# Kernel tuning notes

Hardware: AMD Instinct MI355X
Metric: run time of the kernel (lower is better)

## Reference

```python
import jax, jax.numpy as jnp
import numpy as np


def setup_inputs() -> dict:
    key = jax.random.key(0)
    x = jax.random.normal(key, (8, 16, 256, 256, 3, 3), dtype=jnp.float32)
    return {"x": x, "padding_dim": 1}


def reference(x, padding_dim):
    """Vectorized SPD identity-pad: borders get eye(3), interior copies x.

    x: [B, C, H, W, 3, 3] -> [B, C, H+2p, W+2p, 3, 3]
    Faithful to the original quadruple-nested-loop `padding` function.
    """
    p = padding_dim
    B, C, H, W = x.shape[:4]
    # zero-pad spatial dims, then overwrite border cells with identity
    xp = jnp.pad(x, ((0, 0), (0, 0), (p, p), (p, p), (0, 0), (0, 0)))
    row = jnp.arange(H + 2 * p)
    col = jnp.arange(W + 2 * p)
    # border condition matches: i < p or (H+2p - i) <= p  (i.e. i >= H+p)
    row_border = (row < p) | (row >= H + p)          # [H+2p]
    col_border = (col < p) | (col >= W + p)          # [W+2p]
    border = row_border[:, None] | col_border[None, :]  # [H+2p, W+2p]
    eye = jnp.eye(3, dtype=x.dtype)
    out = jnp.where(border[None, None, :, :, None, None], eye, xp)
    return out
```

## Files before the change

### kernel.cpp

```cpp
#include <hip/hip_runtime.h>


constexpr int B  = 8;
constexpr int C  = 16;
constexpr int H  = 256;
constexpr int W  = 256;
constexpr int HP = 258;
constexpr int WP = 258;

constexpr int       IMGS    = B * C;
constexpr long long ROW_IN  = (long long)W * 9;
constexpr long long IMG_IN  = (long long)H * ROW_IN;
constexpr long long ROW_OUT = (long long)WP * 9;
constexpr long long IMG_OUT = (long long)HP * ROW_OUT;

constexpr int COPY_BLOCKS   = IMGS * H;
constexpr int BORDER_BLOCKS = 2048;
constexpr int       CELLS_PER_IMG = 2 * WP + 2 * H;
constexpr long long BORDER_FLOATS = (long long)IMGS * CELLS_PER_IMG * 9;

__global__ __launch_bounds__(192) void spd_pad_kernel(const float* __restrict__ x,
                                                      float* __restrict__ out) {
    const int blk = blockIdx.x;
    const int tid = threadIdx.x;

    if (blk < COPY_BLOCKS) {
        const int img = blk >> 8;
        const int i   = blk & 255;
        const float4* __restrict__ src =
            reinterpret_cast<const float4*>(x + (long long)img * IMG_IN + (long long)i * ROW_IN);
        float4* __restrict__ dst =
            reinterpret_cast<float4*>(out + (long long)img * IMG_OUT + (long long)(i + 1) * ROW_OUT + 9);
#pragma unroll
        for (int k = 0; k < 3; ++k) {
            const int idx = tid + k * 192;
            dst[idx] = src[idx];
        }
    } else {
        const long long stride = (long long)BORDER_BLOCKS * 192;
        long long t = (long long)(blk - COPY_BLOCKS) * 192 + tid;
        for (; t < BORDER_FLOATS; t += stride) {
            const int       e    = (int)(t % 9);
            const long long cell = t / 9;
            const int       k    = (int)(cell % CELLS_PER_IMG);
            const int       img  = (int)(cell / CELLS_PER_IMG);
            int i, j;
            if (k < WP) {
                i = 0;       j = k;
            } else if (k < 2 * WP) {
                i = HP - 1;  j = k - WP;
            } else if (k < 2 * WP + H) {
                j = 0;       i = k - 2 * WP + 1;
            } else {
                j = WP - 1;  i = k - (2 * WP + H) + 1;
            }
            const float v = (e == 0 || e == 4 || e == 8) ? 1.0f : 0.0f;
            out[(long long)img * IMG_OUT + (long long)i * ROW_OUT + (long long)j * 9 + e] = v;
        }
    }
}

extern "C" void kernel_launch(void* const* d_in, const int* in_sizes, int n_in,
                              void* d_out, int out_size, void* d_ws, size_t ws_size,
                              hipStream_t stream) {
    const float* x   = (const float*)d_in[0];
    float*       out = (float*)d_out;
    spd_pad_kernel<<<dim3(COPY_BLOCKS + BORDER_BLOCKS), dim3(192), 0, stream>>>(x, out);
}
```

Before: 495.8 us.

## Write each output row fully per block with float2 nontemporal stores

Replaces the split copy/border-block scheme with one block per output row. Each block writes the whole padded row, including the identity border cells, using float2 nontemporal stores and nontemporal loads. This removes the separate scattered border writes and the expensive 64-bit div/mod indexing, and gives contiguous full-row writes. The cost is narrower float2 accesses instead of float4, plus per-element branching near the row edges.

New measurement: 504.3 us. No clear change (+1.7%).

```diff
diff --git a/kernel.cpp b/kernel.cpp
--- a/kernel.cpp
+++ b/kernel.cpp
@@ -1,61 +1,57 @@
 #include <hip/hip_runtime.h>
 
 
-constexpr int B  = 8;
-constexpr int C  = 16;
-constexpr int H  = 256;
-constexpr int W  = 256;
-constexpr int HP = 258;
-constexpr int WP = 258;
+constexpr int HP = 258, WP = 258;
+constexpr int ROW_IN  = 256 * 9;
+constexpr int IMG_IN  = 256 * ROW_IN;
+constexpr int ROW_OUT = WP * 9;
+constexpr int IMG_OUT = HP * ROW_OUT;
+constexpr int F2_PER_ROW = ROW_OUT / 2;
+constexpr int IMGS = 8 * 16;
+constexpr int NBLOCKS = IMGS * HP;
 
-constexpr int       IMGS    = B * C;
-constexpr long long ROW_IN  = (long long)W * 9;
-constexpr long long IMG_IN  = (long long)H * ROW_IN;
-constexpr long long ROW_OUT = (long long)WP * 9;
-constexpr long long IMG_OUT = (long long)HP * ROW_OUT;
+typedef float v2f __attribute__((ext_vector_type(2)));
 
-constexpr int COPY_BLOCKS   = IMGS * H;
-constexpr int BORDER_BLOCKS = 2048;
-constexpr int       CELLS_PER_IMG = 2 * WP + 2 * H;
-constexpr long long BORDER_FLOATS = (long long)IMGS * CELLS_PER_IMG * 9;
+__device__ __forceinline__ float eye_val(int e) {
+    return (e == 0 || e == 4 || e == 8) ? 1.0f : 0.0f;
+}
 
-__global__ __launch_bounds__(192) void spd_pad_kernel(const float* __restrict__ x,
-                                                      float* __restrict__ out) {
+__global__ __launch_bounds__(256) void spd_pad_rows(const float* __restrict__ x,
+                                                    float* __restrict__ out) {
     const int blk = blockIdx.x;
-    const int tid = threadIdx.x;
+    const int img = blk / HP;
+    const int i   = blk - img * HP;
+    float* __restrict__ drow = out + img * IMG_OUT + i * ROW_OUT;
+    v2f* __restrict__ drow2 = reinterpret_cast<v2f*>(drow);
 
-    if (blk < COPY_BLOCKS) {
-        const int img = blk >> 8;
-        const int i   = blk & 255;
-        const float4* __restrict__ src =
-            reinterpret_cast<const float4*>(x + (long long)img * IMG_IN + (long long)i * ROW_IN);
-        float4* __restrict__ dst =
-            reinterpret_cast<float4*>(out + (long long)img * IMG_OUT + (long long)(i + 1) * ROW_OUT + 9);
-#pragma unroll
-        for (int k = 0; k < 3; ++k) {
-            const int idx = tid + k * 192;
-            dst[idx] = src[idx];
+    if (i == 0 || i == HP - 1) {
+        for (int idx = threadIdx.x; idx < F2_PER_ROW; idx += 256) {
+            const int c  = idx * 2;
+            const int e0 = c % 9;
+            const int e1 = (e0 == 8) ? 0 : e0 + 1;
+            v2f v;
+            v.x = eye_val(e0);
+            v.y = eye_val(e1);
+            __builtin_nontemporal_store(v, drow2 + idx);
         }
     } else {
-        const long long stride = (long long)BORDER_BLOCKS * 192;
-        long long t = (long long)(blk - COPY_BLOCKS) * 192 + tid;
-        for (; t < BORDER_FLOATS; t += stride) {
-            const int       e    = (int)(t % 9);
-            const long long cell = t / 9;
-            const int       k    = (int)(cell % CELLS_PER_IMG);
-            const int       img  = (int)(cell / CELLS_PER_IMG);
-            int i, j;
-            if (k < WP) {
-                i = 0;       j = k;
-            } else if (k < 2 * WP) {
-                i = HP - 1;  j = k - WP;
-            } else if (k < 2 * WP + H) {
-                j = 0;       i = k - 2 * WP + 1;
+        const float* __restrict__ srow = x + img * IMG_IN + (i - 1) * ROW_IN;
+        for (int idx = threadIdx.x; idx < F2_PER_ROW; idx += 256) {
+            const int c = idx * 2;
+            v2f v;
+            if (c >= 10 && c <= 2310) {
+                v.x = __builtin_nontemporal_load(srow + c - 9);
+                v.y = __builtin_nontemporal_load(srow + c - 8);
             } else {
-                j = WP - 1;  i = k - (2 * WP + H) + 1;
+                const int c1 = c + 1;
+                v.x = (c  < 9) ? eye_val(c)
+                     : (c  >= 2313 ? eye_val(c  - 2313)
+                                   : __builtin_nontemporal_load(srow + c  - 9));
+                v.y = (c1 < 9) ? eye_val(c1)
+                     : (c1 >= 2313 ? eye_val(c1 - 2313)
+                                   : __builtin_nontemporal_load(srow + c1 - 9));
             }
-            const float v = (e == 0 || e == 4 || e == 8) ? 1.0f : 0.0f;
-            out[(long long)img * IMG_OUT + (long long)i * ROW_OUT + (long long)j * 9 + e] = v;
+            __builtin_nontemporal_store(v, drow2 + idx);
         }
     }
 }
@@ -65,5 +61,5 @@
                               hipStream_t stream) {
     const float* x   = (const float*)d_in[0];
     float*       out = (float*)d_out;
-    spd_pad_kernel<<<dim3(COPY_BLOCKS + BORDER_BLOCKS), dim3(192), 0, stream>>>(x, out);
+    spd_pad_rows<<<dim3(NBLOCKS), dim3(256), 0, stream>>>(x, out);
 }
```
